# Kernel tuning notes

Hardware: AMD Instinct MI355X
Metric: run time of the kernel (lower is better)

The kernel has to match this reference:

```python
import jax, jax.numpy as jnp
import numpy as np

H = 4      # attention heads
C = 64     # hidden_dim per head
GAT_SLOPE = 0.2   # PyG GATConv leaky_relu negative_slope
ACT_SLOPE = 0.01  # nn.LeakyReLU / F.leaky_relu default


def gat_layer(x, src, dst, W, a_src, a_dst, b, n):
    # x: [n, F_in] -> h: [n, H, C]
    h = (x @ W).reshape(n, H, C)
    al_s = jnp.einsum('nhc,hc->nh', h, a_src)  # [n, H]
    al_d = jnp.einsum('nhc,hc->nh', h, a_dst)
    e = jax.nn.leaky_relu(al_s[src] + al_d[dst], GAT_SLOPE)  # [E, H]
    # segment softmax over destination nodes (self-loops ensure non-empty segments)
    m = jax.ops.segment_max(e, dst, num_segments=n)
    p = jnp.exp(e - m[dst])
    s = jax.ops.segment_sum(p, dst, num_segments=n)
    alpha = p / s[dst]
    out = jax.ops.segment_sum(h[src] * alpha[:, :, None], dst, num_segments=n)  # [n, H, C]
    return out.reshape(n, H * C) + b


def setup_inputs() -> dict:
    key = jax.random.key(0)
    ks = jax.random.split(key, 24)
    N, E = 102400, 409600
    F_IN, F_OUT = 80, 80
    HC = H * C
    RIN, RHID, ROUT = 60, 512, 60
    def g(k, shape, scale):
        return (jax.random.normal(k, shape, dtype=jnp.float32) * scale)
    inp = {
        'x': g(ks[0], (N, F_IN), 1.0),
        'edge_index': jax.random.randint(ks[1], (2, E), 0, N, dtype=jnp.int64),
        'root_ctx_norm': g(ks[2], (4096, RIN), 1.0),
        'W0': g(ks[3], (F_IN, HC), 0.1), 'a_src0': g(ks[4], (H, C), 0.1), 'a_dst0': g(ks[5], (H, C), 0.1), 'b0': jnp.zeros((HC,), jnp.float32),
        'W1': g(ks[6], (HC, HC), 0.06), 'a_src1': g(ks[7], (H, C), 0.1), 'a_dst1': g(ks[8], (H, C), 0.1), 'b1': jnp.zeros((HC,), jnp.float32),
        'W2': g(ks[9], (HC, HC), 0.06), 'a_src2': g(ks[10], (H, C), 0.1), 'a_dst2': g(ks[11], (H, C), 0.1), 'b2': jnp.zeros((HC,), jnp.float32),
        'fc_w': g(ks[12], (HC, F_OUT), 0.06), 'fc_b': jnp.zeros((F_OUT,), jnp.float32),
        'r_w1': g(ks[13], (RIN, RHID), 0.1), 'r_b1': jnp.zeros((RHID,), jnp.float32),
        'r_w2': g(ks[14], (RHID, RHID), 0.04), 'r_b2': jnp.zeros((RHID,), jnp.float32),
        'r_w3': g(ks[15], (RHID, ROUT), 0.04), 'r_b3': jnp.zeros((ROUT,), jnp.float32),
    }
    return inp


def reference(x, edge_index, root_ctx_norm,
              W0, a_src0, a_dst0, b0,
              W1, a_src1, a_dst1, b1,
              W2, a_src2, a_dst2, b2,
              fc_w, fc_b, r_w1, r_b1, r_w2, r_b2, r_w3, r_b3):
    n = x.shape[0]
    loops = jnp.arange(n, dtype=edge_index.dtype)
    src = jnp.concatenate([edge_index[0], loops])  # PyG add_self_loops=True
    dst = jnp.concatenate([edge_index[1], loops])
    h = gat_layer(x, src, dst, W0, a_src0, a_dst0, b0, n)
    h = jax.nn.leaky_relu(h, ACT_SLOPE)  # dropout is identity in eval
    h = gat_layer(h, src, dst, W1, a_src1, a_dst1, b1, n)
    h = jax.nn.leaky_relu(h, ACT_SLOPE)
    h = gat_layer(h, src, dst, W2, a_src2, a_dst2, b2, n)
    rot = h @ fc_w + fc_b
    r = jax.nn.leaky_relu(root_ctx_norm @ r_w1 + r_b1, ACT_SLOPE)
    r = jax.nn.leaky_relu(r @ r_w2 + r_b2, ACT_SLOPE)
    root_norm = r @ r_w3 + r_b3
    return rot, root_norm
```

## Files before the change

### kernel.cpp

```cpp
#include <hip/hip_runtime.h>
#include <hip/hip_bf16.h>


#define GAT_SLOPE 0.2f
#define ACT_SLOPE 0.01f

typedef unsigned short ushort_t;
typedef __attribute__((ext_vector_type(8))) short bf16x8;
typedef __attribute__((ext_vector_type(8))) unsigned short ushort8v;
typedef __attribute__((ext_vector_type(4))) unsigned short ushort4v;
typedef __attribute__((ext_vector_type(4))) float floatx4;

__device__ __forceinline__ float lrelu(float x, float s) {
    return fmaxf(x, s * x);
}

__device__ __forceinline__ ushort_t f2bf(float f) {
    union { float f; unsigned u; } x; x.f = f;
    unsigned r = x.u + 0x7FFF + ((x.u >> 16) & 1);
    return (ushort_t)(r >> 16);
}

__device__ __forceinline__ float bf2f(ushort_t u) {
    union { unsigned u; float f; } x; x.u = ((unsigned)u) << 16;
    return x.f;
}

__global__ void detect_fmt(const int* __restrict__ raw, int nwords, int* flag) {
    __shared__ int nz;
    if (threadIdx.x == 0) nz = 0;
    __syncthreads();
    int lim = nwords < 4096 ? nwords : 4096;
    for (int i = threadIdx.x * 2 + 1; i < lim; i += 512)
        if (raw[i] != 0) atomicAdd(&nz, 1);
    __syncthreads();
    if (threadIdx.x == 0) *flag = (nz == 0) ? 1 : 0;
}

__global__ void zero2(int* __restrict__ a, int* __restrict__ b, int n) {
    int i = blockIdx.x * blockDim.x + threadIdx.x;
    if (i < n) { a[i] = 0; b[i] = 0; }
}

__global__ void convert_count(const int* __restrict__ raw, int E,
                              const int* __restrict__ flag,
                              int* __restrict__ idx32, int* __restrict__ counts) {
    int i = blockIdx.x * blockDim.x + threadIdx.x;
    if (i >= E) return;
    int f = *flag;
    int s = f ? raw[2 * i] : raw[i];
    int d = f ? raw[2 * (E + i)] : raw[E + i];
    idx32[i] = s;
    idx32[E + i] = d;
    atomicAdd(&counts[d], 1);
}

__global__ void scan_block(const int* __restrict__ counts, int* __restrict__ inc,
                           int* __restrict__ blockSums, int N) {
    __shared__ int sh[256];
    int i = blockIdx.x * 256 + threadIdx.x;
    int v = (i < N) ? counts[i] : 0;
    sh[threadIdx.x] = v;
    __syncthreads();
    for (int off = 1; off < 256; off <<= 1) {
        int t = (threadIdx.x >= off) ? sh[threadIdx.x - off] : 0;
        __syncthreads();
        sh[threadIdx.x] += t;
        __syncthreads();
    }
    if (i < N) inc[i] = sh[threadIdx.x];
    if (threadIdx.x == 255) blockSums[blockIdx.x] = sh[255];
}

__global__ void scan_sums(int* __restrict__ blockSums, int nb, int* __restrict__ row_ptr) {
    __shared__ int sh[512];
    int v = ((int)threadIdx.x < nb) ? blockSums[threadIdx.x] : 0;
    sh[threadIdx.x] = v;
    __syncthreads();
    for (int off = 1; off < 512; off <<= 1) {
        int t = (threadIdx.x >= off) ? sh[threadIdx.x - off] : 0;
        __syncthreads();
        sh[threadIdx.x] += t;
        __syncthreads();
    }
    if ((int)threadIdx.x < nb) blockSums[threadIdx.x] = sh[threadIdx.x];
    if (threadIdx.x == 0) row_ptr[0] = 0;
}

__global__ void scan_add(const int* __restrict__ inc, const int* __restrict__ blockSums,
                         int* __restrict__ row_ptr, int N) {
    int i = blockIdx.x * 256 + threadIdx.x;
    if (i < N) row_ptr[i + 1] = inc[i] + (blockIdx.x > 0 ? blockSums[blockIdx.x - 1] : 0);
}

__global__ void edge_fill(const int* __restrict__ src, const int* __restrict__ dst, int E,
                          const int* __restrict__ row_ptr, int* __restrict__ cursor,
                          int* __restrict__ col) {
    int i = blockIdx.x * blockDim.x + threadIdx.x;
    if (i < E) {
        int d = dst[i];
        int pos = row_ptr[d] + atomicAdd(&cursor[d], 1);
        col[pos] = src[i];
    }
}

__global__ void convert_padrow(const float* __restrict__ in, ushort_t* __restrict__ out,
                               int M, int Kr, int Kp) {
    int i = blockIdx.x * blockDim.x + threadIdx.x;
    if (i >= M * Kp) return;
    int r = i / Kp, c = i - r * Kp;
    out[i] = f2bf((c < Kr) ? in[(size_t)r * Kr + c] : 0.f);
}

struct WConv { const float* in; ushort_t* out; int Kp, Kr, N, Npad, blkOff; };
struct WConvArr { WConv e[7]; int n; };

__global__ void convert_w_multi(WConvArr a) {
    int b = blockIdx.x;
    int ei = 0;
    for (int k = 1; k < a.n; k++)
        if (b >= a.e[k].blkOff) ei = k;
    WConv w = a.e[ei];
    int i = (b - w.blkOff) * 256 + threadIdx.x;
    if (i >= w.Npad * w.Kp) return;
    int n = i / w.Kp, k = i - n * w.Kp;
    float v = (n < w.N && k < w.Kr) ? w.in[(size_t)k * w.N + n] : 0.f;
    w.out[i] = f2bf(v);
}

__global__ __launch_bounds__(256) void gemm_gat(
    const ushort_t* __restrict__ A, const ushort_t* __restrict__ Bt,
    const float* __restrict__ a_src, const float* __restrict__ a_dst,
    ushort_t* __restrict__ Hbf, float* __restrict__ al_s, float* __restrict__ al_d,
    int M, int K) {
    __shared__ __align__(16) ushort_t As[2][128 * 32];
    __shared__ __align__(16) ushort_t Bs[2][128 * 32];
    int t = threadIdx.x;
    int wave = t >> 6, lane = t & 63;
    int wm = (wave >> 1) << 6;
    int wn = (wave & 1) << 6;
    int rowBase = blockIdx.y << 7;
    int colBase = blockIdx.x << 7;
    int lrow = lane & 15, lquad = lane >> 4;
    floatx4 acc[4][4];
#pragma unroll
    for (int i = 0; i < 4; i++)
#pragma unroll
        for (int j = 0; j < 4; j++) acc[i][j] = (floatx4){0.f, 0.f, 0.f, 0.f};

    int c0 = wave * 64 + lane;
    const ushort_t* gA0 = A + (size_t)(rowBase + (c0 >> 2)) * K + ((c0 & 3) << 3);
    const ushort_t* gB0 = Bt + (size_t)(colBase + (c0 >> 2)) * K + ((c0 & 3) << 3);
    int c1 = 256 + c0;
    const ushort_t* gA1 = A + (size_t)(rowBase + (c1 >> 2)) * K + ((c1 & 3) << 3);
    const ushort_t* gB1 = Bt + (size_t)(colBase + (c1 >> 2)) * K + ((c1 & 3) << 3);
    const int wsl0 = (wave * 64 + lane) * 8;
    const int wsl1 = (256 + wave * 64 + lane) * 8;

    const int nt = K >> 5;
    ushort8v rA0, rA1, rB0, rB1;
#define LOADR(tt)                                     \
    do {                                              \
        int k0_ = (tt) << 5;                          \
        rA0 = *(const ushort8v*)(gA0 + k0_);          \
        rA1 = *(const ushort8v*)(gA1 + k0_);          \
        rB0 = *(const ushort8v*)(gB0 + k0_);          \
        rB1 = *(const ushort8v*)(gB1 + k0_);          \
    } while (0)
#define WRITER(b)                                     \
    do {                                              \
        *(ushort8v*)(&As[b][wsl0]) = rA0;             \
        *(ushort8v*)(&As[b][wsl1]) = rA1;             \
        *(ushort8v*)(&Bs[b][wsl0]) = rB0;             \
        *(ushort8v*)(&Bs[b][wsl1]) = rB1;             \
    } while (0)

    LOADR(0);
    WRITER(0);
    LOADR(1);
    asm volatile("s_waitcnt lgkmcnt(0)" ::: "memory");
    __builtin_amdgcn_s_barrier();

    for (int kt = 0; kt < nt; ++kt) {
        int b = kt & 1;
        if (kt + 1 < nt) WRITER(b ^ 1);
        if (kt + 2 < nt) LOADR(kt + 2);
        bf16x8 af[4], bfv[4];
#pragma unroll
        for (int i = 0; i < 4; i++)
            af[i] = *(const bf16x8*)(&As[b][(wm + i * 16 + lrow) * 32 + lquad * 8]);
#pragma unroll
        for (int j = 0; j < 4; j++)
            bfv[j] = *(const bf16x8*)(&Bs[b][(wn + j * 16 + lrow) * 32 + lquad * 8]);
#pragma unroll
        for (int i = 0; i < 4; i++)
#pragma unroll
            for (int j = 0; j < 4; j++)
                acc[i][j] = __builtin_amdgcn_mfma_f32_16x16x32_bf16(af[i], bfv[j],
                                                                    acc[i][j], 0, 0, 0);
        asm volatile("s_waitcnt lgkmcnt(0)" ::: "memory");
        __builtin_amdgcn_s_barrier();
    }
#undef LOADR
#undef WRITER

    int head = (colBase + wn) >> 6;
    float avs[4], avd[4];
#pragma unroll
    for (int j = 0; j < 4; j++) {
        avs[j] = a_src[head * 64 + j * 16 + lrow];
        avd[j] = a_dst[head * 64 + j * 16 + lrow];
    }
#pragma unroll
    for (int i = 0; i < 4; i++) {
#pragma unroll
        for (int r = 0; r < 4; r++) {
            float ps = 0.f, pd = 0.f;
#pragma unroll
            for (int j = 0; j < 4; j++) {
                ps += acc[i][j][r] * avs[j];
                pd += acc[i][j][r] * avd[j];
            }
#pragma unroll
            for (int off = 1; off < 16; off <<= 1) {
                ps += __shfl_xor(ps, off);
                pd += __shfl_xor(pd, off);
            }
            if (lrow == 0) {
                int gr = rowBase + wm + i * 16 + lquad * 4 + r;
                al_s[gr * 4 + head] = ps;
                al_d[gr * 4 + head] = pd;
            }
        }
        int grb = rowBase + wm + i * 16 + lquad * 4;
#pragma unroll
        for (int j = 0; j < 4; j++) {
            int gc = colBase + wn + j * 16 + lrow;
#pragma unroll
            for (int r = 0; r < 4; r++)
                Hbf[(size_t)(grb + r) * 256 + gc] = f2bf(acc[i][j][r]);
        }
    }
}

__global__ __launch_bounds__(256) void gemm_plain(
    const ushort_t* __restrict__ A, const ushort_t* __restrict__ Bt,
    const float* __restrict__ bias, void* __restrict__ Cout,
    int M, int N, int K, int act, float slope, int outBf) {
    __shared__ __align__(16) ushort_t As[2][128 * 32];
    __shared__ __align__(16) ushort_t Bs[2][128 * 32];
    int t = threadIdx.x;
    int wave = t >> 6, lane = t & 63;
    int wm = (wave >> 1) << 6;
    int wn = (wave & 1) << 6;
    int rowBase = blockIdx.y << 7;
    int colBase = blockIdx.x << 7;
    int lrow = lane & 15, lquad = lane >> 4;
    floatx4 acc[4][4];
#pragma unroll
    for (int i = 0; i < 4; i++)
#pragma unroll
        for (int j = 0; j < 4; j++) acc[i][j] = (floatx4){0.f, 0.f, 0.f, 0.f};

    int c0 = wave * 64 + lane;
    const ushort_t* gA0 = A + (size_t)(rowBase + (c0 >> 2)) * K + ((c0 & 3) << 3);
    const ushort_t* gB0 = Bt + (size_t)(colBase + (c0 >> 2)) * K + ((c0 & 3) << 3);
    int c1 = 256 + c0;
    const ushort_t* gA1 = A + (size_t)(rowBase + (c1 >> 2)) * K + ((c1 & 3) << 3);
    const ushort_t* gB1 = Bt + (size_t)(colBase + (c1 >> 2)) * K + ((c1 & 3) << 3);
    const int wsl0 = (wave * 64 + lane) * 8;
    const int wsl1 = (256 + wave * 64 + lane) * 8;

    const int nt = K >> 5;
    ushort8v rA0, rA1, rB0, rB1;
#define LOADR(tt)                                     \
    do {                                              \
        int k0_ = (tt) << 5;                          \
        rA0 = *(const ushort8v*)(gA0 + k0_);          \
        rA1 = *(const ushort8v*)(gA1 + k0_);          \
        rB0 = *(const ushort8v*)(gB0 + k0_);          \
        rB1 = *(const ushort8v*)(gB1 + k0_);          \
    } while (0)
#define WRITER(b)                                     \
    do {                                              \
        *(ushort8v*)(&As[b][wsl0]) = rA0;             \
        *(ushort8v*)(&As[b][wsl1]) = rA1;             \
        *(ushort8v*)(&Bs[b][wsl0]) = rB0;             \
        *(ushort8v*)(&Bs[b][wsl1]) = rB1;             \
    } while (0)

    LOADR(0);
    WRITER(0);
    LOADR(1);
    asm volatile("s_waitcnt lgkmcnt(0)" ::: "memory");
    __builtin_amdgcn_s_barrier();

    for (int kt = 0; kt < nt; ++kt) {
        int b = kt & 1;
        if (kt + 1 < nt) WRITER(b ^ 1);
        if (kt + 2 < nt) LOADR(kt + 2);
        bf16x8 af[4], bfv[4];
#pragma unroll
        for (int i = 0; i < 4; i++)
            af[i] = *(const bf16x8*)(&As[b][(wm + i * 16 + lrow) * 32 + lquad * 8]);
#pragma unroll
        for (int j = 0; j < 4; j++)
            bfv[j] = *(const bf16x8*)(&Bs[b][(wn + j * 16 + lrow) * 32 + lquad * 8]);
#pragma unroll
        for (int i = 0; i < 4; i++)
#pragma unroll
            for (int j = 0; j < 4; j++)
                acc[i][j] = __builtin_amdgcn_mfma_f32_16x16x32_bf16(af[i], bfv[j],
                                                                    acc[i][j], 0, 0, 0);
        asm volatile("s_waitcnt lgkmcnt(0)" ::: "memory");
        __builtin_amdgcn_s_barrier();
    }
#undef LOADR
#undef WRITER

#pragma unroll
    for (int i = 0; i < 4; i++) {
        int gr = rowBase + wm + i * 16 + lquad * 4;
#pragma unroll
        for (int j = 0; j < 4; j++) {
            int gc = colBase + wn + j * 16 + lrow;
            if (gc >= N) continue;
            float b = bias ? bias[gc] : 0.f;
#pragma unroll
            for (int r = 0; r < 4; r++) {
                float v = acc[i][j][r] + b;
                if (act) v = lrelu(v, slope);
                if (outBf)
                    ((ushort_t*)Cout)[(size_t)(gr + r) * N + gc] = f2bf(v);
                else
                    ((float*)Cout)[(size_t)(gr + r) * N + gc] = v;
            }
        }
    }
}

__global__ __launch_bounds__(256) void gat_agg(
    const ushort_t* __restrict__ h_bf, const float* __restrict__ al_s,
    const float* __restrict__ al_d, const int* __restrict__ row_ptr,
    const int* __restrict__ col, const float* __restrict__ bias,
    ushort_t* __restrict__ out_bf, int N, int act, float slope) {
    int wid = (blockIdx.x * 256 + threadIdx.x) >> 6;
    int lane = threadIdx.x & 63;
    int half = lane >> 5;
    int lane8 = lane & 31;
    int n = wid * 2 + half;
    if (n >= N) return;
    int head = lane8 >> 3;
    int idx4 = n * 4 + head;
    float ad = al_d[idx4];
    const ushort8v* h8 = (const ushort8v*)h_bf;
    float p = __expf(lrelu(al_s[idx4] + ad, GAT_SLOPE));
    ushort8v hv = h8[(size_t)n * 32 + lane8];
    float s = p;
    float acc[8];
#pragma unroll
    for (int c = 0; c < 8; c++) acc[c] = p * bf2f(hv[c]);
    int beg = row_ptr[n], end = row_ptr[n + 1];
    for (int i = beg; i < end; i += 4) {
        int cnt = end - i;
        int sn0 = col[i];
        int sn1 = (cnt > 1) ? col[i + 1] : sn0;
        int sn2 = (cnt > 2) ? col[i + 2] : sn0;
        int sn3 = (cnt > 3) ? col[i + 3] : sn0;
        ushort8v h0 = h8[(size_t)sn0 * 32 + lane8];
        ushort8v h1 = h8[(size_t)sn1 * 32 + lane8];
        ushort8v h2 = h8[(size_t)sn2 * 32 + lane8];
        ushort8v h3 = h8[(size_t)sn3 * 32 + lane8];
        float a0 = al_s[sn0 * 4 + head];
        float a1 = al_s[sn1 * 4 + head];
        float a2 = al_s[sn2 * 4 + head];
        float a3 = al_s[sn3 * 4 + head];
        float p0 = __expf(lrelu(a0 + ad, GAT_SLOPE));
#pragma unroll
        for (int c = 0; c < 8; c++) acc[c] += p0 * bf2f(h0[c]);
        s += p0;
        if (cnt > 1) {
            float p1 = __expf(lrelu(a1 + ad, GAT_SLOPE));
#pragma unroll
            for (int c = 0; c < 8; c++) acc[c] += p1 * bf2f(h1[c]);
            s += p1;
        }
        if (cnt > 2) {
            float p2 = __expf(lrelu(a2 + ad, GAT_SLOPE));
#pragma unroll
            for (int c = 0; c < 8; c++) acc[c] += p2 * bf2f(h2[c]);
            s += p2;
        }
        if (cnt > 3) {
            float p3 = __expf(lrelu(a3 + ad, GAT_SLOPE));
#pragma unroll
            for (int c = 0; c < 8; c++) acc[c] += p3 * bf2f(h3[c]);
            s += p3;
        }
    }
    float rs = 1.f / s;
    const float4* b4 = (const float4*)bias;
    float4 b0 = b4[lane8 * 2];
    float4 b1 = b4[lane8 * 2 + 1];
    float bv[8] = {b0.x, b0.y, b0.z, b0.w, b1.x, b1.y, b1.z, b1.w};
    ushort8v o;
#pragma unroll
    for (int c = 0; c < 8; c++) {
        float v = acc[c] * rs + bv[c];
        if (act) v = lrelu(v, slope);
        o[c] = f2bf(v);
    }
    ((ushort8v*)out_bf)[(size_t)n * 32 + lane8] = o;
}

extern "C" void kernel_launch(void* const* d_in, const int* in_sizes, int n_in,
                              void* d_out, int out_size, void* d_ws, size_t ws_size,
                              hipStream_t stream) {
    const float* x        = (const float*)d_in[0];
    const int*   rawEdge  = (const int*)d_in[1];
    const float* rootCtx  = (const float*)d_in[2];
    const float* W[3]     = {(const float*)d_in[3], (const float*)d_in[7], (const float*)d_in[11]};
    const float* aS[3]    = {(const float*)d_in[4], (const float*)d_in[8], (const float*)d_in[12]};
    const float* aD[3]    = {(const float*)d_in[5], (const float*)d_in[9], (const float*)d_in[13]};
    const float* bb[3]    = {(const float*)d_in[6], (const float*)d_in[10], (const float*)d_in[14]};
    const float* fc_w     = (const float*)d_in[15];
    const float* fc_b     = (const float*)d_in[16];
    const float* r_w1     = (const float*)d_in[17];
    const float* r_b1     = (const float*)d_in[18];
    const float* r_w2     = (const float*)d_in[19];
    const float* r_b2     = (const float*)d_in[20];
    const float* r_w3     = (const float*)d_in[21];
    const float* r_b3     = (const float*)d_in[22];

    const int N  = in_sizes[0] / 80;
    const int E  = in_sizes[1] / 2;
    const int R  = in_sizes[2] / 60;
    const int N4 = N * 4;

    float* outRot  = (float*)d_out;
    float* outRoot = (float*)d_out + (size_t)N * 80;

    size_t off = 0;
    auto carve = [&](size_t bytes) -> void* {
        off = (off + 255) & ~(size_t)255;
        void* p = (char*)d_ws + off;
        off += bytes;
        return p;
    };
    int*      flag      = (int*)carve(4);
    int*      idx32     = (int*)carve((size_t)2 * E * 4);
    int*      counts    = (int*)carve((size_t)N * 4);
    int*      cursor    = (int*)carve((size_t)N * 4);
    int*      row_ptr   = (int*)carve((size_t)(N + 1) * 4);
    int*      incArr    = (int*)carve((size_t)N * 4);
    int*      blockSums = (int*)carve(512 * 4);
    int*      colArr    = (int*)carve((size_t)E * 4);
    float*    al_s      = (float*)carve((size_t)N4 * 4);
    float*    al_d      = (float*)carve((size_t)N4 * 4);
    ushort_t* h_bf      = (ushort_t*)carve((size_t)N * 256 * 2);
    ushort_t* agg_bf    = (ushort_t*)carve((size_t)N * 256 * 2);
    ushort_t* x_bf      = (ushort_t*)carve((size_t)N * 96 * 2);
    ushort_t* rc_bf     = (ushort_t*)carve((size_t)R * 64 * 2);
    ushort_t* t1_bf     = (ushort_t*)carve((size_t)R * 512 * 2);
    ushort_t* t2_bf     = (ushort_t*)carve((size_t)R * 512 * 2);
    ushort_t* Wt0       = (ushort_t*)carve((size_t)256 * 96 * 2);
    ushort_t* Wt1       = (ushort_t*)carve((size_t)256 * 256 * 2);
    ushort_t* Wt2       = (ushort_t*)carve((size_t)256 * 256 * 2);
    ushort_t* fcWt      = (ushort_t*)carve((size_t)128 * 256 * 2);
    ushort_t* rW1t      = (ushort_t*)carve((size_t)512 * 64 * 2);
    ushort_t* rWt2      = (ushort_t*)carve((size_t)512 * 512 * 2);
    ushort_t* rWt3      = (ushort_t*)carve((size_t)128 * 512 * 2);

    const int nb = (N + 255) / 256;
    dim3 blk(256);

    detect_fmt<<<1, 256, 0, stream>>>(rawEdge, 2 * E, flag);
    zero2<<<(N + 255) / 256, blk, 0, stream>>>(counts, cursor, N);
    convert_count<<<(E + 255) / 256, blk, 0, stream>>>(rawEdge, E, flag, idx32, counts);
    const int* srcArr = idx32;
    const int* dstArr = idx32 + E;
    scan_block<<<nb, 256, 0, stream>>>(counts, incArr, blockSums, N);
    scan_sums<<<1, 512, 0, stream>>>(blockSums, nb, row_ptr);
    scan_add<<<nb, 256, 0, stream>>>(incArr, blockSums, row_ptr, N);
    edge_fill<<<(E + 255) / 256, blk, 0, stream>>>(srcArr, dstArr, E, row_ptr, cursor, colArr);

    {
        WConvArr wa;
        auto mk = [&](int i, const float* in, ushort_t* out, int Kp, int Kr, int Nn, int Npad,
                      int blkOff) {
            wa.e[i] = WConv{in, out, Kp, Kr, Nn, Npad, blkOff};
        };
        int boff = 0;
        auto nblk = [](int Npad, int Kp) { return (Npad * Kp + 255) / 256; };
        mk(0, W[0], Wt0, 96, 80, 256, 256, boff);   boff += nblk(256, 96);
        mk(1, W[1], Wt1, 256, 256, 256, 256, boff); boff += nblk(256, 256);
        mk(2, W[2], Wt2, 256, 256, 256, 256, boff); boff += nblk(256, 256);
        mk(3, fc_w, fcWt, 256, 256, 80, 128, boff); boff += nblk(128, 256);
        mk(4, r_w1, rW1t, 64, 60, 512, 512, boff);  boff += nblk(512, 64);
        mk(5, r_w2, rWt2, 512, 512, 512, 512, boff); boff += nblk(512, 512);
        mk(6, r_w3, rWt3, 512, 512, 60, 128, boff);  boff += nblk(128, 512);
        wa.n = 7;
        convert_w_multi<<<boff, blk, 0, stream>>>(wa);
    }
    convert_padrow<<<(N * 96 + 255) / 256, blk, 0, stream>>>(x, x_bf, N, 80, 96);
    convert_padrow<<<(R * 64 + 255) / 256, blk, 0, stream>>>(rootCtx, rc_bf, R, 60, 64);

    const int aggBlocks = (N / 2 + 3) / 4;
    const ushort_t* curA = x_bf;
    int curK = 96;
    for (int l = 0; l < 3; l++) {
        dim3 g1(2, N / 128);
        gemm_gat<<<g1, blk, 0, stream>>>(curA, l == 0 ? Wt0 : (l == 1 ? Wt1 : Wt2),
                                         aS[l], aD[l], h_bf, al_s, al_d, N, curK);
        int act = (l < 2) ? 1 : 0;
        gat_agg<<<aggBlocks, blk, 0, stream>>>(h_bf, al_s, al_d, row_ptr,
                                               colArr, bb[l], agg_bf, N,
                                               act, ACT_SLOPE);
        curA = agg_bf;
        curK = 256;
    }

    {
        dim3 g(1, N / 128);
        gemm_plain<<<g, blk, 0, stream>>>(agg_bf, fcWt, fc_b, outRot, N, 80, 256,
                                          0, 0.f, 0);
    }
    {
        dim3 g1(512 / 128, R / 128);
        gemm_plain<<<g1, blk, 0, stream>>>(rc_bf, rW1t, r_b1, t1_bf, R, 512, 64,
                                           1, ACT_SLOPE, 1);
        dim3 g2(512 / 128, R / 128);
        gemm_plain<<<g2, blk, 0, stream>>>(t1_bf, rWt2, r_b2, t2_bf, R, 512, 512,
                                           1, ACT_SLOPE, 1);
        dim3 g3(1, R / 128);
        gemm_plain<<<g3, blk, 0, stream>>>(t2_bf, rWt3, r_b3, outRoot, R, 60, 512,
                                           0, 0.f, 0);
    }
}
```

Measured before the change: 510.8 us.

## Fold root-context MLP GEMMs into the GAT projection launches as extra blocks

Each of the three root MLP layers now runs as extra tail blocks inside the per-layer gemm_gat launch, selected by blockIdx.y beyond the main node rows. This removes three separate small kernel launches and lets the MLP work fill idle compute units alongside the larger GAT projection. The shared GEMM pipeline moves into a macro reused by both branches. The cost is a larger kernel with more branching and possibly higher register pressure, plus a dependency chain: each MLP layer now waits for the previous GAT layer's launch.

```diff
diff --git a/kernel.cpp b/kernel.cpp
--- a/kernel.cpp
+++ b/kernel.cpp
@@ -8,7 +8,6 @@
 typedef unsigned short ushort_t;
 typedef __attribute__((ext_vector_type(8))) short bf16x8;
 typedef __attribute__((ext_vector_type(8))) unsigned short ushort8v;
-typedef __attribute__((ext_vector_type(4))) unsigned short ushort4v;
 typedef __attribute__((ext_vector_type(4))) float floatx4;
 
 __device__ __forceinline__ float lrelu(float x, float s) {
@@ -128,37 +127,6 @@
     w.out[i] = f2bf(v);
 }
 
-__global__ __launch_bounds__(256) void gemm_gat(
-    const ushort_t* __restrict__ A, const ushort_t* __restrict__ Bt,
-    const float* __restrict__ a_src, const float* __restrict__ a_dst,
-    ushort_t* __restrict__ Hbf, float* __restrict__ al_s, float* __restrict__ al_d,
-    int M, int K) {
-    __shared__ __align__(16) ushort_t As[2][128 * 32];
-    __shared__ __align__(16) ushort_t Bs[2][128 * 32];
-    int t = threadIdx.x;
-    int wave = t >> 6, lane = t & 63;
-    int wm = (wave >> 1) << 6;
-    int wn = (wave & 1) << 6;
-    int rowBase = blockIdx.y << 7;
-    int colBase = blockIdx.x << 7;
-    int lrow = lane & 15, lquad = lane >> 4;
-    floatx4 acc[4][4];
-#pragma unroll
-    for (int i = 0; i < 4; i++)
-#pragma unroll
-        for (int j = 0; j < 4; j++) acc[i][j] = (floatx4){0.f, 0.f, 0.f, 0.f};
-
-    int c0 = wave * 64 + lane;
-    const ushort_t* gA0 = A + (size_t)(rowBase + (c0 >> 2)) * K + ((c0 & 3) << 3);
-    const ushort_t* gB0 = Bt + (size_t)(colBase + (c0 >> 2)) * K + ((c0 & 3) << 3);
-    int c1 = 256 + c0;
-    const ushort_t* gA1 = A + (size_t)(rowBase + (c1 >> 2)) * K + ((c1 & 3) << 3);
-    const ushort_t* gB1 = Bt + (size_t)(colBase + (c1 >> 2)) * K + ((c1 & 3) << 3);
-    const int wsl0 = (wave * 64 + lane) * 8;
-    const int wsl1 = (256 + wave * 64 + lane) * 8;
-
-    const int nt = K >> 5;
-    ushort8v rA0, rA1, rB0, rB1;
 #define LOADR(tt)                                     \
     do {                                              \
         int k0_ = (tt) << 5;                          \
@@ -167,6 +135,7 @@
         rB0 = *(const ushort8v*)(gB0 + k0_);          \
         rB1 = *(const ushort8v*)(gB1 + k0_);          \
     } while (0)
+
 #define WRITER(b)                                     \
     do {                                              \
         *(ushort8v*)(&As[b][wsl0]) = rA0;             \
@@ -175,70 +144,140 @@
         *(ushort8v*)(&Bs[b][wsl1]) = rB1;             \
     } while (0)
 
-    LOADR(0);
-    WRITER(0);
-    LOADR(1);
-    asm volatile("s_waitcnt lgkmcnt(0)" ::: "memory");
-    __builtin_amdgcn_s_barrier();
-
-    for (int kt = 0; kt < nt; ++kt) {
-        int b = kt & 1;
-        if (kt + 1 < nt) WRITER(b ^ 1);
-        if (kt + 2 < nt) LOADR(kt + 2);
-        bf16x8 af[4], bfv[4];
-#pragma unroll
-        for (int i = 0; i < 4; i++)
-            af[i] = *(const bf16x8*)(&As[b][(wm + i * 16 + lrow) * 32 + lquad * 8]);
-#pragma unroll
-        for (int j = 0; j < 4; j++)
-            bfv[j] = *(const bf16x8*)(&Bs[b][(wn + j * 16 + lrow) * 32 + lquad * 8]);
-#pragma unroll
-        for (int i = 0; i < 4; i++)
-#pragma unroll
-            for (int j = 0; j < 4; j++)
-                acc[i][j] = __builtin_amdgcn_mfma_f32_16x16x32_bf16(af[i], bfv[j],
-                                                                    acc[i][j], 0, 0, 0);
-        asm volatile("s_waitcnt lgkmcnt(0)" ::: "memory");
-        __builtin_amdgcn_s_barrier();
-    }
-#undef LOADR
-#undef WRITER
-
-    int head = (colBase + wn) >> 6;
-    float avs[4], avd[4];
-#pragma unroll
-    for (int j = 0; j < 4; j++) {
-        avs[j] = a_src[head * 64 + j * 16 + lrow];
-        avd[j] = a_dst[head * 64 + j * 16 + lrow];
-    }
-#pragma unroll
-    for (int i = 0; i < 4; i++) {
-#pragma unroll
-        for (int r = 0; r < 4; r++) {
-            float ps = 0.f, pd = 0.f;
+#define GEMM_PIPELINE(NT)                                                        \
+    ushort8v rA0, rA1, rB0, rB1;                                                 \
+    LOADR(0);                                                                    \
+    WRITER(0);                                                                   \
+    LOADR(1);                                                                    \
+    asm volatile("s_waitcnt lgkmcnt(0)" ::: "memory");                           \
+    __builtin_amdgcn_s_barrier();                                                \
+    for (int kt = 0; kt < (NT); ++kt) {                                          \
+        int b = kt & 1;                                                          \
+        if (kt + 1 < (NT)) WRITER(b ^ 1);                                        \
+        if (kt + 2 < (NT)) LOADR(kt + 2);                                        \
+        bf16x8 af[4], bfv[4];                                                    \
+        _Pragma("unroll")                                                        \
+        for (int i = 0; i < 4; i++)                                              \
+            af[i] = *(const bf16x8*)(&As[b][(wm + i * 16 + lrow) * 32            \
+                                            + lquad * 8]);                       \
+        _Pragma("unroll")                                                        \
+        for (int j = 0; j < 4; j++)                                              \
+            bfv[j] = *(const bf16x8*)(&Bs[b][(wn + j * 16 + lrow) * 32           \
+                                             + lquad * 8]);                      \
+        _Pragma("unroll")                                                        \
+        for (int i = 0; i < 4; i++)                                              \
+            _Pragma("unroll")                                                    \
+            for (int j = 0; j < 4; j++)                                          \
+                acc[i][j] = __builtin_amdgcn_mfma_f32_16x16x32_bf16(             \
+                    af[i], bfv[j], acc[i][j], 0, 0, 0);                          \
+        asm volatile("s_waitcnt lgkmcnt(0)" ::: "memory");                       \
+        __builtin_amdgcn_s_barrier();                                            \
+    }
+
+__global__ __launch_bounds__(256) void gemm_gat(
+    const ushort_t* __restrict__ A, const ushort_t* __restrict__ Bt,
+    const float* __restrict__ a_src, const float* __restrict__ a_dst,
+    ushort_t* __restrict__ Hbf, float* __restrict__ al_s, float* __restrict__ al_d,
+    int K, int yMain,
+    const ushort_t* __restrict__ xA, const ushort_t* __restrict__ xBt,
+    const float* __restrict__ xBias, void* __restrict__ xC,
+    int xN, int xK, int xGX, int xCnt, int xAct, float xSlope, int xOutBf) {
+    __shared__ __align__(16) ushort_t As[2][128 * 32];
+    __shared__ __align__(16) ushort_t Bs[2][128 * 32];
+    int t = threadIdx.x;
+    int wave = t >> 6, lane = t & 63;
+    int wm = (wave >> 1) << 6;
+    int wn = (wave & 1) << 6;
+    int lrow = lane & 15, lquad = lane >> 4;
+    const int wsl0 = (wave * 64 + lane) * 8;
+    const int wsl1 = (256 + wave * 64 + lane) * 8;
+    int c0 = wave * 64 + lane;
+    int c1 = 256 + c0;
+
+    floatx4 acc[4][4];
+#pragma unroll
+    for (int i = 0; i < 4; i++)
+#pragma unroll
+        for (int j = 0; j < 4; j++) acc[i][j] = (floatx4){0.f, 0.f, 0.f, 0.f};
+
+    if ((int)blockIdx.y < yMain) {
+        int rowBase = blockIdx.y << 7;
+        int colBase = blockIdx.x << 7;
+        const ushort_t* gA0 = A + (size_t)(rowBase + (c0 >> 2)) * K + ((c0 & 3) << 3);
+        const ushort_t* gB0 = Bt + (size_t)(colBase + (c0 >> 2)) * K + ((c0 & 3) << 3);
+        const ushort_t* gA1 = A + (size_t)(rowBase + (c1 >> 2)) * K + ((c1 & 3) << 3);
+        const ushort_t* gB1 = Bt + (size_t)(colBase + (c1 >> 2)) * K + ((c1 & 3) << 3);
+        const int nt = K >> 5;
+        GEMM_PIPELINE(nt);
+
+        int head = (colBase + wn) >> 6;
+        float avs[4], avd[4];
+#pragma unroll
+        for (int j = 0; j < 4; j++) {
+            avs[j] = a_src[head * 64 + j * 16 + lrow];
+            avd[j] = a_dst[head * 64 + j * 16 + lrow];
+        }
+#pragma unroll
+        for (int i = 0; i < 4; i++) {
+#pragma unroll
+            for (int r = 0; r < 4; r++) {
+                float ps = 0.f, pd = 0.f;
+#pragma unroll
+                for (int j = 0; j < 4; j++) {
+                    ps += acc[i][j][r] * avs[j];
+                    pd += acc[i][j][r] * avd[j];
+                }
+#pragma unroll
+                for (int off = 1; off < 16; off <<= 1) {
+                    ps += __shfl_xor(ps, off);
+                    pd += __shfl_xor(pd, off);
+                }
+                if (lrow == 0) {
+                    int gr = rowBase + wm + i * 16 + lquad * 4 + r;
+                    al_s[gr * 4 + head] = ps;
+                    al_d[gr * 4 + head] = pd;
+                }
+            }
+            int grb = rowBase + wm + i * 16 + lquad * 4;
 #pragma unroll
             for (int j = 0; j < 4; j++) {
-                ps += acc[i][j][r] * avs[j];
-                pd += acc[i][j][r] * avd[j];
+                int gc = colBase + wn + j * 16 + lrow;
+#pragma unroll
+                for (int r = 0; r < 4; r++)
+                    Hbf[(size_t)(grb + r) * 256 + gc] = f2bf(acc[i][j][r]);
             }
-#pragma unroll
-            for (int off = 1; off < 16; off <<= 1) {
-                ps += __shfl_xor(ps, off);
-                pd += __shfl_xor(pd, off);
+        }
+    } else {
+        int id = (blockIdx.y - yMain) * 2 + blockIdx.x;
+        if (id >= xCnt) return;
+        int bxp = id % xGX, byp = id / xGX;
+        int rowBase = byp << 7;
+        int colBase = bxp << 7;
+        const ushort_t* gA0 = xA + (size_t)(rowBase + (c0 >> 2)) * xK + ((c0 & 3) << 3);
+        const ushort_t* gB0 = xBt + (size_t)(colBase + (c0 >> 2)) * xK + ((c0 & 3) << 3);
+        const ushort_t* gA1 = xA + (size_t)(rowBase + (c1 >> 2)) * xK + ((c1 & 3) << 3);
+        const ushort_t* gB1 = xBt + (size_t)(colBase + (c1 >> 2)) * xK + ((c1 & 3) << 3);
+        const int nt = xK >> 5;
+        GEMM_PIPELINE(nt);
+
+#pragma unroll
+        for (int i = 0; i < 4; i++) {
+            int gr = rowBase + wm + i * 16 + lquad * 4;
+#pragma unroll
+            for (int j = 0; j < 4; j++) {
+                int gc = colBase + wn + j * 16 + lrow;
+                if (gc >= xN) continue;
+                float b = xBias ? xBias[gc] : 0.f;
+#pragma unroll
+                for (int r = 0; r < 4; r++) {
+                    float v = acc[i][j][r] + b;
+                    if (xAct) v = lrelu(v, xSlope);
+                    if (xOutBf)
+                        ((ushort_t*)xC)[(size_t)(gr + r) * xN + gc] = f2bf(v);
+                    else
+                        ((float*)xC)[(size_t)(gr + r) * xN + gc] = v;
+                }
             }
-            if (lrow == 0) {
-                int gr = rowBase + wm + i * 16 + lquad * 4 + r;
-                al_s[gr * 4 + head] = ps;
-                al_d[gr * 4 + head] = pd;
-            }
-        }
-        int grb = rowBase + wm + i * 16 + lquad * 4;
-#pragma unroll
-        for (int j = 0; j < 4; j++) {
-            int gc = colBase + wn + j * 16 + lrow;
-#pragma unroll
-            for (int r = 0; r < 4; r++)
-                Hbf[(size_t)(grb + r) * 256 + gc] = f2bf(acc[i][j][r]);
         }
     }
 }
@@ -272,51 +311,7 @@
     const int wsl1 = (256 + wave * 64 + lane) * 8;
 
     const int nt = K >> 5;
-    ushort8v rA0, rA1, rB0, rB1;
-#define LOADR(tt)                                     \
-    do {                                              \
-        int k0_ = (tt) << 5;                          \
-        rA0 = *(const ushort8v*)(gA0 + k0_);          \
-        rA1 = *(const ushort8v*)(gA1 + k0_);          \
-        rB0 = *(const ushort8v*)(gB0 + k0_);          \
-        rB1 = *(const ushort8v*)(gB1 + k0_);          \
-    } while (0)
-#define WRITER(b)                                     \
-    do {                                              \
-        *(ushort8v*)(&As[b][wsl0]) = rA0;             \
-        *(ushort8v*)(&As[b][wsl1]) = rA1;             \
-        *(ushort8v*)(&Bs[b][wsl0]) = rB0;             \
-        *(ushort8v*)(&Bs[b][wsl1]) = rB1;             \
-    } while (0)
-
-    LOADR(0);
-    WRITER(0);
-    LOADR(1);
-    asm volatile("s_waitcnt lgkmcnt(0)" ::: "memory");
-    __builtin_amdgcn_s_barrier();
-
-    for (int kt = 0; kt < nt; ++kt) {
-        int b = kt & 1;
-        if (kt + 1 < nt) WRITER(b ^ 1);
-        if (kt + 2 < nt) LOADR(kt + 2);
-        bf16x8 af[4], bfv[4];
-#pragma unroll
-        for (int i = 0; i < 4; i++)
-            af[i] = *(const bf16x8*)(&As[b][(wm + i * 16 + lrow) * 32 + lquad * 8]);
-#pragma unroll
-        for (int j = 0; j < 4; j++)
-            bfv[j] = *(const bf16x8*)(&Bs[b][(wn + j * 16 + lrow) * 32 + lquad * 8]);
-#pragma unroll
-        for (int i = 0; i < 4; i++)
-#pragma unroll
-            for (int j = 0; j < 4; j++)
-                acc[i][j] = __builtin_amdgcn_mfma_f32_16x16x32_bf16(af[i], bfv[j],
-                                                                    acc[i][j], 0, 0, 0);
-        asm volatile("s_waitcnt lgkmcnt(0)" ::: "memory");
-        __builtin_amdgcn_s_barrier();
-    }
-#undef LOADR
-#undef WRITER
+    GEMM_PIPELINE(nt);
 
 #pragma unroll
     for (int i = 0; i < 4; i++) {
@@ -506,12 +501,28 @@
     convert_padrow<<<(R * 64 + 255) / 256, blk, 0, stream>>>(rootCtx, rc_bf, R, 60, 64);
 
     const int aggBlocks = (N / 2 + 3) / 4;
+    const int yMain = N / 128;
     const ushort_t* curA = x_bf;
     int curK = 96;
+    const int mlpGY = R / 128;
     for (int l = 0; l < 3; l++) {
-        dim3 g1(2, N / 128);
+        const ushort_t* xA  = (l == 0) ? rc_bf : (l == 1 ? t1_bf : t2_bf);
+        const ushort_t* xBt = (l == 0) ? rW1t : (l == 1 ? rWt2 : rWt3);
+        const float*    xB  = (l == 0) ? r_b1 : (l == 1 ? r_b2 : r_b3);
+        void*           xC  = (l == 0) ? (void*)t1_bf : (l == 1 ? (void*)t2_bf : (void*)outRoot);
+        int xN   = (l == 2) ? 60 : 512;
+        int xK   = (l == 0) ? 64 : 512;
+        int xGX  = (l == 2) ? 1 : 4;
+        int xCnt = xGX * mlpGY;
+        int xAct = (l == 2) ? 0 : 1;
+        int xOutBf = (l == 2) ? 0 : 1;
+        int extraY = (xCnt + 1) / 2;
+        dim3 g1(2, yMain + extraY);
         gemm_gat<<<g1, blk, 0, stream>>>(curA, l == 0 ? Wt0 : (l == 1 ? Wt1 : Wt2),
-                                         aS[l], aD[l], h_bf, al_s, al_d, N, curK);
+                                         aS[l], aD[l], h_bf, al_s, al_d,
+                                         curK, yMain,
+                                         xA, xBt, xB, xC,
+                                         xN, xK, xGX, xCnt, xAct, ACT_SLOPE, xOutBf);
         int act = (l < 2) ? 1 : 0;
         gat_agg<<<aggBlocks, blk, 0, stream>>>(h_bf, al_s, al_d, row_ptr,
                                                colArr, bb[l], agg_bf, N,
@@ -525,15 +536,4 @@
         gemm_plain<<<g, blk, 0, stream>>>(agg_bf, fcWt, fc_b, outRot, N, 80, 256,
                                           0, 0.f, 0);
     }
-    {
-        dim3 g1(512 / 128, R / 128);
-        gemm_plain<<<g1, blk, 0, stream>>>(rc_bf, rW1t, r_b1, t1_bf, R, 512, 64,
-                                           1, ACT_SLOPE, 1);
-        dim3 g2(512 / 128, R / 128);
-        gemm_plain<<<g2, blk, 0, stream>>>(t1_bf, rWt2, r_b2, t2_bf, R, 512, 512,
-                                           1, ACT_SLOPE, 1);
-        dim3 g3(1, R / 128);
-        gemm_plain<<<g3, blk, 0, stream>>>(t2_bf, rWt3, r_b3, outRoot, R, 60, 512,
-                                           0, 0.f, 0);
-    }
-}
+}
```

Measured after the change: 481.3 us. 1.06x faster.
